# Kernel tuning notes

Measured on AMD Instinct MI355X. Metric: run time of the kernel, lower is better.

Reference implementation:

```python
import jax, jax.numpy as jnp
import numpy as np

N_NODES = 50000
N_EDGES = 300000
IN_FEATS = 128
N_HIDDEN = 64
N_HEADS = 4
N_CLASSES = 47
NEG_SLOPE = 0.2


def setup_inputs() -> dict:
    key = jax.random.key(0)
    ks = jax.random.split(key, 16)
    s = 0.1
    inp = {
        "x": jax.random.normal(ks[0], (N_NODES, IN_FEATS), jnp.float32),
        "src": jax.random.randint(ks[1], (N_EDGES,), 0, N_NODES, jnp.int64 if jax.config.jax_enable_x64 else jnp.int32),
        "dst": jax.random.randint(ks[2], (N_EDGES,), 0, N_NODES, jnp.int64 if jax.config.jax_enable_x64 else jnp.int32),
        # layer 1: in_feats -> (heads, hidden)
        "W1": jax.random.normal(ks[3], (IN_FEATS, N_HEADS * N_HIDDEN), jnp.float32) * s,
        "al1": jax.random.normal(ks[4], (N_HEADS, N_HIDDEN), jnp.float32) * s,
        "ar1": jax.random.normal(ks[5], (N_HEADS, N_HIDDEN), jnp.float32) * s,
        "b1": jnp.zeros((N_HEADS * N_HIDDEN,), jnp.float32),
        # layer 2: heads*hidden -> (heads, hidden)
        "W2": jax.random.normal(ks[6], (N_HEADS * N_HIDDEN, N_HEADS * N_HIDDEN), jnp.float32) * s,
        "al2": jax.random.normal(ks[7], (N_HEADS, N_HIDDEN), jnp.float32) * s,
        "ar2": jax.random.normal(ks[8], (N_HEADS, N_HIDDEN), jnp.float32) * s,
        "b2": jnp.zeros((N_HEADS * N_HIDDEN,), jnp.float32),
        # layer 3: heads*hidden -> (1, n_classes)
        "W3": jax.random.normal(ks[9], (N_HEADS * N_HIDDEN, N_CLASSES), jnp.float32) * s,
        "al3": jax.random.normal(ks[10], (1, N_CLASSES), jnp.float32) * s,
        "ar3": jax.random.normal(ks[11], (1, N_CLASSES), jnp.float32) * s,
        "b3": jnp.zeros((N_CLASSES,), jnp.float32),
    }
    return inp


def gat_conv(h, src, dst, W, al, ar, b, n_nodes):
    """DGL GATConv (shared src/dst projection, edge-softmax over dst)."""
    H, D = al.shape
    feat = (h @ W).reshape(n_nodes, H, D)              # [N,H,D]
    el = jnp.sum(feat * al[None], axis=-1)             # [N,H]
    er = jnp.sum(feat * ar[None], axis=-1)             # [N,H]
    e = jax.nn.leaky_relu(el[src] + er[dst], NEG_SLOPE)  # [E,H]
    emax = jax.ops.segment_max(e, dst, num_segments=n_nodes)  # [N,H]
    emax = jnp.where(jnp.isfinite(emax), emax, 0.0)    # empty segments
    ee = jnp.exp(e - emax[dst])                        # [E,H]
    denom = jax.ops.segment_sum(ee, dst, num_segments=n_nodes)  # [N,H]
    alpha = ee / jnp.maximum(denom[dst], 1e-9)         # [E,H]
    msg = feat[src] * alpha[..., None]                 # [E,H,D]
    out = jax.ops.segment_sum(msg, dst, num_segments=n_nodes)   # [N,H,D]
    return out + b.reshape(1, H, D)


def reference(x, src, dst, W1, al1, ar1, b1, W2, al2, ar2, b2, W3, al3, ar3, b3):
    n = x.shape[0]
    h = gat_conv(x, src, dst, W1, al1, ar1, b1, n).reshape(n, -1)  # flatten heads
    h = gat_conv(h, src, dst, W2, al2, ar2, b2, n).reshape(n, -1)
    h = gat_conv(h, src, dst, W3, al3, ar3, b3, n)                 # [N,1,C]
    return h.mean(axis=1)                                          # [N,C]
```

## Files before the change

### kernel.cpp

```cpp
#include <hip/hip_runtime.h>
#include <cstddef>

#define GAT_N 50000
#define GAT_E 300000
#define SCAN_B 256

typedef short bf16x8 __attribute__((ext_vector_type(8)));
typedef float f32x4  __attribute__((ext_vector_type(4)));
typedef unsigned int u32;

__device__ __forceinline__ ushort f2bf(float f) {
    unsigned u = __float_as_uint(f);
    return (ushort)((u + 0x7fffu + ((u >> 16) & 1u)) >> 16);
}
__device__ __forceinline__ float bf2f(ushort h) {
    return __uint_as_float((unsigned)h << 16);
}

__device__ __forceinline__ void gload16(const ushort* g, ushort* l) {
    __builtin_amdgcn_global_load_lds(
        (const __attribute__((address_space(1))) u32*)g,
        (__attribute__((address_space(3))) u32*)l, 16, 0, 0);
}


__global__ __launch_bounds__(256) void zero_ints(int* __restrict__ a, int n) {
    int i = blockIdx.x * blockDim.x + threadIdx.x;
    int stride = gridDim.x * blockDim.x;
    for (; i < n; i += stride) a[i] = 0;
}

__global__ __launch_bounds__(256) void count_k(
    const int* __restrict__ dst, int* __restrict__ cnt, int E)
{
    int e = blockIdx.x * blockDim.x + threadIdx.x;
    if (e < E) atomicAdd(&cnt[dst[e]], 1);
}

__global__ __launch_bounds__(256) void csr_partial(
    const int* __restrict__ cnt, int* __restrict__ partials, int N, int chunk)
{
    __shared__ int red[256];
    int b = blockIdx.x, t = threadIdx.x;
    int s = 0;
    for (int i = t; i < chunk; i += 256) {
        int idx = b * chunk + i;
        if (idx < N) s += cnt[idx];
    }
    red[t] = s;
    __syncthreads();
    for (int off = 128; off > 0; off >>= 1) {
        if (t < off) red[t] += red[t + off];
        __syncthreads();
    }
    if (t == 0) partials[b] = red[0];
}

__global__ __launch_bounds__(SCAN_B) void csr_scanp(
    int* __restrict__ partials, int* __restrict__ rowptr, int N)
{
    __shared__ int sc[SCAN_B];
    int t = threadIdx.x;
    int v = partials[t];
    sc[t] = v;
    __syncthreads();
    for (int off = 1; off < SCAN_B; off <<= 1) {
        int u = (t >= off) ? sc[t - off] : 0;
        __syncthreads();
        sc[t] += u;
        __syncthreads();
    }
    partials[t] = sc[t] - v;
    if (t == SCAN_B - 1) rowptr[N] = sc[t];
}

__global__ __launch_bounds__(256) void csr_write(
    const int* __restrict__ cnt, const int* __restrict__ partials,
    int* __restrict__ rowptr, int N, int chunk)
{
    __shared__ int sc[256];
    int b = blockIdx.x, t = threadIdx.x;
    int idx = b * chunk + t;
    int v = (t < chunk && idx < N) ? cnt[idx] : 0;
    sc[t] = v;
    __syncthreads();
    for (int off = 1; off < 256; off <<= 1) {
        int u = (t >= off) ? sc[t - off] : 0;
        __syncthreads();
        sc[t] += u;
        __syncthreads();
    }
    if (t < chunk && idx < N) rowptr[idx] = partials[b] + sc[t] - v;
}

__global__ __launch_bounds__(256) void scatter_k(
    const int* __restrict__ src, const int* __restrict__ dst,
    const int* __restrict__ rowptr, int* __restrict__ cursor,
    int* __restrict__ ssrc, int* __restrict__ sdst, int E)
{
    int e = blockIdx.x * blockDim.x + threadIdx.x;
    if (e >= E) return;
    int d = dst[e];
    int p = rowptr[d] + atomicAdd(&cursor[d], 1);
    ssrc[p] = src[e];
    sdst[p] = d;
}


__global__ __launch_bounds__(256) void convert_x(
    const float* __restrict__ x, ushort* __restrict__ Xh, ushort* __restrict__ Xl,
    long total4)
{
    long i = (long)blockIdx.x * blockDim.x + threadIdx.x;
    long stride = (long)gridDim.x * blockDim.x;
    for (; i < total4; i += stride) {
        float4 v = *(const float4*)(x + i * 4);
        ushort4 h, lo;
        h.x = f2bf(v.x); lo.x = f2bf(v.x - bf2f(h.x));
        h.y = f2bf(v.y); lo.y = f2bf(v.y - bf2f(h.y));
        h.z = f2bf(v.z); lo.z = f2bf(v.z - bf2f(h.z));
        h.w = f2bf(v.w); lo.w = f2bf(v.w - bf2f(h.w));
        *(ushort4*)(Xh + i * 4) = h;
        *(ushort4*)(Xl + i * 4) = lo;
    }
}

__global__ __launch_bounds__(256) void convert_w(
    const float* __restrict__ W, ushort* __restrict__ Wth, ushort* __restrict__ Wtl,
    int K, int M, int Mp)
{
    int idx = blockIdx.x * blockDim.x + threadIdx.x;
    if (idx >= Mp * K) return;
    int c = idx / K, k = idx - c * K;
    float v = (c < M) ? W[(size_t)k * M + c] : 0.f;
    ushort h = f2bf(v);
    Wth[idx] = h;
    Wtl[idx] = f2bf(v - bf2f(h));
}


__global__ __launch_bounds__(256) void gemm_feat(
    const ushort* __restrict__ Ah, const ushort* __restrict__ Al,
    const ushort* __restrict__ Wh, const ushort* __restrict__ Wl,
    const float* __restrict__ alw, const float* __restrict__ arw,
    float* __restrict__ feat, float* __restrict__ el, float* __restrict__ er,
    int N, int K, int M, int H, int D, int ldF)
{
    __shared__ ushort lds[2 * 16384];

    const int m0 = blockIdx.x * 128;
    const int n0 = blockIdx.y * 128;
    const int t = threadIdx.x;
    const int w = t >> 6, lane = t & 63;
    const int lr = lane & 15, lg = lane >> 4;
    const int wrb = (w >> 1) * 4;
    const int wcb = (w & 1) * 4;
    const int NK = K >> 5;

    const ushort* srcp[8];
    u32 lbase[8];
    #pragma unroll
    for (int l = 0; l < 8; ++l) {
        int ub = l * 256 + w * 64;
        int u = ub + lane;
        int region = u >> 9;
        int v = u & 511;
        int rowblk = v >> 6, kc = (v >> 4) & 3, rc = v & 15;
        const ushort* s;
        if (region < 2) {
            int grow = m0 + rowblk * 16 + rc;
            grow = grow < N ? grow : N - 1;
            s = (region ? Al : Ah) + (size_t)grow * K + kc * 8;
        } else {
            int gcol = n0 + rowblk * 16 + rc;
            s = ((region & 1) ? Wl : Wh) + (size_t)gcol * K + kc * 8;
        }
        srcp[l] = s;
        lbase[l] = (u32)(ub * 8);
    }

    f32x4 acc[4][4] = {};

    #pragma unroll
    for (int l = 0; l < 8; ++l) {
        gload16(srcp[l], &lds[lbase[l]]);
        srcp[l] += 32;
    }
    __syncthreads();

    int cur = 0;
    for (int kt = 0; kt < NK; ++kt) {
        if (kt + 1 < NK) {
            int nb = (cur ^ 1) * 16384;
            #pragma unroll
            for (int l = 0; l < 8; ++l) {
                gload16(srcp[l], &lds[nb + lbase[l]]);
                srcp[l] += 32;
            }
        }
        const ushort* buf = lds + cur * 16384;
        bf16x8 a_h[4], a_l[4];
        #pragma unroll
        for (int fi = 0; fi < 4; ++fi) {
            int aidx = ((wrb + fi) * 4 + lg) * 128 + lr * 8;
            a_h[fi] = *(const bf16x8*)&buf[aidx];
            a_l[fi] = *(const bf16x8*)&buf[4096 + aidx];
        }
        #pragma unroll
        for (int fj = 0; fj < 4; ++fj) {
            int bidx = ((wcb + fj) * 4 + lg) * 128 + lr * 8;
            bf16x8 b_h = *(const bf16x8*)&buf[8192 + bidx];
            bf16x8 b_l = *(const bf16x8*)&buf[12288 + bidx];
            #pragma unroll
            for (int fi = 0; fi < 4; ++fi) {
                acc[fi][fj] = __builtin_amdgcn_mfma_f32_16x16x32_bf16(a_h[fi], b_h, acc[fi][fj], 0, 0, 0);
                acc[fi][fj] = __builtin_amdgcn_mfma_f32_16x16x32_bf16(a_l[fi], b_h, acc[fi][fj], 0, 0, 0);
                acc[fi][fj] = __builtin_amdgcn_mfma_f32_16x16x32_bf16(a_h[fi], b_l, acc[fi][fj], 0, 0, 0);
            }
        }
        __syncthreads();
        cur ^= 1;
    }

    #pragma unroll
    for (int fi = 0; fi < 4; ++fi) {
        #pragma unroll
        for (int q = 0; q < 4; ++q) {
            int row = m0 + (w >> 1) * 64 + fi * 16 + 4 * lg + q;
            if (row < N) {
                #pragma unroll
                for (int fj = 0; fj < 4; ++fj) {
                    int col = n0 + (w & 1) * 64 + fj * 16 + lr;
                    if (col < M) feat[(size_t)row * ldF + col] = acc[fi][fj][q];
                }
            }
        }
    }

    const int head = (n0 + (w & 1) * 64) / D;
    if (head < H) {
        float alv[4], arv[4];
        #pragma unroll
        for (int fj = 0; fj < 4; ++fj) {
            int col = n0 + (w & 1) * 64 + fj * 16 + lr;
            alv[fj] = (col < M) ? alw[col] : 0.f;
            arv[fj] = (col < M) ? arw[col] : 0.f;
        }
        #pragma unroll
        for (int fi = 0; fi < 4; ++fi) {
            #pragma unroll
            for (int q = 0; q < 4; ++q) {
                float s1 = 0.f, s2 = 0.f;
                #pragma unroll
                for (int fj = 0; fj < 4; ++fj) {
                    s1 = fmaf(acc[fi][fj][q], alv[fj], s1);
                    s2 = fmaf(acc[fi][fj][q], arv[fj], s2);
                }
                #pragma unroll
                for (int mask = 1; mask <= 8; mask <<= 1) {
                    s1 += __shfl_xor(s1, mask);
                    s2 += __shfl_xor(s2, mask);
                }
                int row = m0 + (w >> 1) * 64 + fi * 16 + 4 * lg + q;
                if (lr == 0 && row < N) {
                    el[(size_t)row * H + head] = s1;
                    er[(size_t)row * H + head] = s2;
                }
            }
        }
    }
}


__global__ __launch_bounds__(256) void edge_score4(
    const int* __restrict__ ssrc, const int* __restrict__ sdst,
    const float* __restrict__ el, const float* __restrict__ er,
    float* __restrict__ sc, int E)
{
    int p = blockIdx.x * blockDim.x + threadIdx.x;
    if (p >= E) return;
    int s = ssrc[p], d = sdst[p];
    float4 a = *(const float4*)(el + (size_t)s * 4);
    float4 b = *(const float4*)(er + (size_t)d * 4);
    float4 v;
    v.x = a.x + b.x; v.x = v.x > 0.f ? v.x : 0.2f * v.x;
    v.y = a.y + b.y; v.y = v.y > 0.f ? v.y : 0.2f * v.y;
    v.z = a.z + b.z; v.z = v.z > 0.f ? v.z : 0.2f * v.z;
    v.w = a.w + b.w; v.w = v.w > 0.f ? v.w : 0.2f * v.w;
    *(float4*)(sc + (size_t)p * 4) = v;
}

__global__ __launch_bounds__(256) void edge_score1(
    const int* __restrict__ ssrc, const int* __restrict__ sdst,
    const float* __restrict__ el, const float* __restrict__ er,
    float* __restrict__ sc, int E)
{
    int p = blockIdx.x * blockDim.x + threadIdx.x;
    if (p >= E) return;
    float v = el[ssrc[p]] + er[sdst[p]];
    sc[p] = v > 0.f ? v : 0.2f * v;
}


__global__ __launch_bounds__(256) void node_aggr256(
    const int* __restrict__ rowptr, const int* __restrict__ ssrc,
    const float* __restrict__ sc, const float* __restrict__ feat,
    const float* __restrict__ bias,
    ushort* __restrict__ Ah_out, ushort* __restrict__ Al_out, int N)
{
    int wid = blockIdx.x * 4 + (threadIdx.x >> 6);
    int na = wid * 2;
    if (na >= N) return;
    int nb = na + 1;
    bool hb = nb < N;
    int lane = threadIdx.x & 63;
    int h = lane >> 4, sub = lane & 15;
    int begA = rowptr[na], endA = rowptr[na + 1];
    int begB = 0, endB = 0;
    if (hb) { begB = rowptr[nb]; endB = rowptr[nb + 1]; }

    float ma = -__builtin_inff(), mb = -__builtin_inff();
    for (int j = begA + sub; j < endA; j += 16) ma = fmaxf(ma, sc[(size_t)j * 4 + h]);
    for (int j = begB + sub; j < endB; j += 16) mb = fmaxf(mb, sc[(size_t)j * 4 + h]);
    #pragma unroll
    for (int mask = 1; mask <= 8; mask <<= 1) {
        ma = fmaxf(ma, __shfl_xor(ma, mask));
        mb = fmaxf(mb, __shfl_xor(mb, mask));
    }

    float dena = 0.f, denb = 0.f;
    for (int j = begA + sub; j < endA; j += 16) dena += __expf(sc[(size_t)j * 4 + h] - ma);
    for (int j = begB + sub; j < endB; j += 16) denb += __expf(sc[(size_t)j * 4 + h] - mb);
    #pragma unroll
    for (int mask = 1; mask <= 8; mask <<= 1) {
        dena += __shfl_xor(dena, mask);
        denb += __shfl_xor(denb, mask);
    }
    float invA = 1.f / fmaxf(dena, 1e-9f);
    float invB = 1.f / fmaxf(denb, 1e-9f);

    int degA = endA - begA, degB = endB - begB;
    int dmax = degA > degB ? degA : degB;

    float a0 = 0.f, a1 = 0.f, a2 = 0.f, a3 = 0.f;
    float b0 = 0.f, b1 = 0.f, b2 = 0.f, b3 = 0.f;
    for (int k = 0; k < dmax; k += 2) {
        bool v0 = k < degA,     v1 = k + 1 < degA;
        bool v2 = k < degB,     v3 = k + 1 < degB;
        int i0 = v0 ? begA + k     : 0;
        int i1 = v1 ? begA + k + 1 : 0;
        int i2 = v2 ? begB + k     : 0;
        int i3 = v3 ? begB + k + 1 : 0;
        int s0 = ssrc[i0], s1 = ssrc[i1], s2 = ssrc[i2], s3 = ssrc[i3];
        float w0 = v0 ? __expf(sc[(size_t)i0 * 4 + h] - ma) : 0.f;
        float w1 = v1 ? __expf(sc[(size_t)i1 * 4 + h] - ma) : 0.f;
        float w2 = v2 ? __expf(sc[(size_t)i2 * 4 + h] - mb) : 0.f;
        float w3 = v3 ? __expf(sc[(size_t)i3 * 4 + h] - mb) : 0.f;
        float4 f0 = *(const float4*)(feat + (size_t)s0 * 256 + lane * 4);
        float4 f1 = *(const float4*)(feat + (size_t)s1 * 256 + lane * 4);
        float4 f2 = *(const float4*)(feat + (size_t)s2 * 256 + lane * 4);
        float4 f3 = *(const float4*)(feat + (size_t)s3 * 256 + lane * 4);
        a0 = fmaf(w0, f0.x, fmaf(w1, f1.x, a0));
        a1 = fmaf(w0, f0.y, fmaf(w1, f1.y, a1));
        a2 = fmaf(w0, f0.z, fmaf(w1, f1.z, a2));
        a3 = fmaf(w0, f0.w, fmaf(w1, f1.w, a3));
        b0 = fmaf(w2, f2.x, fmaf(w3, f3.x, b0));
        b1 = fmaf(w2, f2.y, fmaf(w3, f3.y, b1));
        b2 = fmaf(w2, f2.z, fmaf(w3, f3.z, b2));
        b3 = fmaf(w2, f2.w, fmaf(w3, f3.w, b3));
    }

    float bs0 = bias[lane * 4 + 0], bs1 = bias[lane * 4 + 1];
    float bs2 = bias[lane * 4 + 2], bs3 = bias[lane * 4 + 3];
    {
        float v0 = fmaf(a0, invA, bs0), v1 = fmaf(a1, invA, bs1);
        float v2 = fmaf(a2, invA, bs2), v3 = fmaf(a3, invA, bs3);
        ushort4 hh, lo;
        hh.x = f2bf(v0); lo.x = f2bf(v0 - bf2f(hh.x));
        hh.y = f2bf(v1); lo.y = f2bf(v1 - bf2f(hh.y));
        hh.z = f2bf(v2); lo.z = f2bf(v2 - bf2f(hh.z));
        hh.w = f2bf(v3); lo.w = f2bf(v3 - bf2f(hh.w));
        *(ushort4*)(Ah_out + (size_t)na * 256 + lane * 4) = hh;
        *(ushort4*)(Al_out + (size_t)na * 256 + lane * 4) = lo;
    }
    if (hb) {
        float v0 = fmaf(b0, invB, bs0), v1 = fmaf(b1, invB, bs1);
        float v2 = fmaf(b2, invB, bs2), v3 = fmaf(b3, invB, bs3);
        ushort4 hh, lo;
        hh.x = f2bf(v0); lo.x = f2bf(v0 - bf2f(hh.x));
        hh.y = f2bf(v1); lo.y = f2bf(v1 - bf2f(hh.y));
        hh.z = f2bf(v2); lo.z = f2bf(v2 - bf2f(hh.z));
        hh.w = f2bf(v3); lo.w = f2bf(v3 - bf2f(hh.w));
        *(ushort4*)(Ah_out + (size_t)nb * 256 + lane * 4) = hh;
        *(ushort4*)(Al_out + (size_t)nb * 256 + lane * 4) = lo;
    }
}

__global__ __launch_bounds__(256) void node_aggr47(
    const int* __restrict__ rowptr, const int* __restrict__ ssrc,
    const float* __restrict__ sc, const float* __restrict__ feat,
    const float* __restrict__ bias, float* __restrict__ out, int N)
{
    int n = blockIdx.x * 4 + (threadIdx.x >> 6);
    if (n >= N) return;
    int lane = threadIdx.x & 63;
    int beg = rowptr[n], end = rowptr[n + 1];

    float m = -__builtin_inff();
    for (int j = beg + lane; j < end; j += 64)
        m = fmaxf(m, sc[j]);
    #pragma unroll
    for (int mask = 1; mask <= 32; mask <<= 1)
        m = fmaxf(m, __shfl_xor(m, mask));

    float denom = 0.f;
    for (int j = beg + lane; j < end; j += 64)
        denom += __expf(sc[j] - m);
    #pragma unroll
    for (int mask = 1; mask <= 32; mask <<= 1)
        denom += __shfl_xor(denom, mask);

    float inv = 1.f / fmaxf(denom, 1e-9f);
    float acc = 0.f;
    int j = beg;
    for (; j + 4 <= end; j += 4) {
        int s0 = ssrc[j + 0], s1 = ssrc[j + 1], s2 = ssrc[j + 2], s3 = ssrc[j + 3];
        float w0 = __expf(sc[j + 0] - m);
        float w1 = __expf(sc[j + 1] - m);
        float w2 = __expf(sc[j + 2] - m);
        float w3 = __expf(sc[j + 3] - m);
        float f0 = (lane < 47) ? feat[(size_t)s0 * 48 + lane] : 0.f;
        float f1 = (lane < 47) ? feat[(size_t)s1 * 48 + lane] : 0.f;
        float f2 = (lane < 47) ? feat[(size_t)s2 * 48 + lane] : 0.f;
        float f3 = (lane < 47) ? feat[(size_t)s3 * 48 + lane] : 0.f;
        acc = fmaf(w0, f0, fmaf(w1, f1, fmaf(w2, f2, fmaf(w3, f3, acc))));
    }
    for (; j < end; ++j) {
        float wgt = __expf(sc[j] - m);
        int s = ssrc[j];
        float f = (lane < 47) ? feat[(size_t)s * 48 + lane] : 0.f;
        acc = fmaf(wgt, f, acc);
    }
    if (lane < 47)
        out[(size_t)n * 47 + lane] = fmaf(acc, inv, bias[lane]);
}


extern "C" void kernel_launch(void* const* d_in, const int* in_sizes, int n_in,
                              void* d_out, int out_size, void* d_ws, size_t ws_size,
                              hipStream_t stream) {
    const float* x   = (const float*)d_in[0];
    const int*   src = (const int*)d_in[1];
    const int*   dst = (const int*)d_in[2];
    const float* W1  = (const float*)d_in[3];
    const float* al1 = (const float*)d_in[4];
    const float* ar1 = (const float*)d_in[5];
    const float* b1  = (const float*)d_in[6];
    const float* W2  = (const float*)d_in[7];
    const float* al2 = (const float*)d_in[8];
    const float* ar2 = (const float*)d_in[9];
    const float* b2  = (const float*)d_in[10];
    const float* W3  = (const float*)d_in[11];
    const float* al3 = (const float*)d_in[12];
    const float* ar3 = (const float*)d_in[13];
    const float* b3  = (const float*)d_in[14];
    float* out = (float*)d_out;

    const int N = GAT_N, E = GAT_E;
    const int chunk = (N + SCAN_B - 1) / SCAN_B;

    char* wsb = (char*)d_ws;
    size_t o = 0;
    float*  feat  = (float*)(wsb + o);  o += (size_t)N * 256 * 4;
    ushort* Ah    = (ushort*)(wsb + o); o += (size_t)N * 256 * 2;
    ushort* Al    = (ushort*)(wsb + o); o += (size_t)N * 256 * 2;
    float*  el    = (float*)(wsb + o);  o += (size_t)N * 4 * 4;
    float*  er    = (float*)(wsb + o);  o += (size_t)N * 4 * 4;
    int* rowptr   = (int*)(wsb + o);    o += (size_t)(N + 1) * 4;
    int* cnt      = (int*)(wsb + o);    o += (size_t)N * 4;
    int* cursor   = (int*)(wsb + o);    o += (size_t)N * 4;
    int* ssrc     = (int*)(wsb + o);    o += (size_t)E * 4;
    int* sdst     = (int*)(wsb + o);    o += (size_t)E * 4;
    float* scbuf  = (float*)(wsb + o);  o += (size_t)E * 4 * 4;
    int* partials = (int*)(wsb + o);    o += (size_t)SCAN_B * 4;
    ushort* Wt1h  = (ushort*)(wsb + o); o += (size_t)256 * 128 * 2;
    ushort* Wt1l  = (ushort*)(wsb + o); o += (size_t)256 * 128 * 2;
    ushort* Wt2h  = (ushort*)(wsb + o); o += (size_t)256 * 256 * 2;
    ushort* Wt2l  = (ushort*)(wsb + o); o += (size_t)256 * 256 * 2;
    ushort* Wt3h  = (ushort*)(wsb + o); o += (size_t)128 * 256 * 2;
    ushort* Wt3l  = (ushort*)(wsb + o); o += (size_t)128 * 256 * 2;
    ushort* Xh = Ah;
    ushort* Xl = Al;

    dim3 blk(256);
    int gE = (E + 255) / 256;
    int gN = (N + 3) / 4;
    int gN2 = ((N + 1) / 2 + 3) / 4;
    dim3 gemmG((N + 127) / 128, 2);
    dim3 gemmG3((N + 127) / 128, 1);

    zero_ints<<<64, blk, 0, stream>>>(cnt, 2 * N);
    count_k<<<gE, blk, 0, stream>>>(dst, cnt, E);
    csr_partial<<<SCAN_B, blk, 0, stream>>>(cnt, partials, N, chunk);
    csr_scanp<<<1, SCAN_B, 0, stream>>>(partials, rowptr, N);
    csr_write<<<SCAN_B, blk, 0, stream>>>(cnt, partials, rowptr, N, chunk);
    scatter_k<<<gE, blk, 0, stream>>>(src, dst, rowptr, cursor, ssrc, sdst, E);

    convert_x<<<2048, blk, 0, stream>>>(x, Xh, Xl, (long)N * 128 / 4);
    convert_w<<<(256 * 128 + 255) / 256, blk, 0, stream>>>(W1, Wt1h, Wt1l, 128, 256, 256);
    convert_w<<<(256 * 256 + 255) / 256, blk, 0, stream>>>(W2, Wt2h, Wt2l, 256, 256, 256);
    convert_w<<<(128 * 256 + 255) / 256, blk, 0, stream>>>(W3, Wt3h, Wt3l, 256, 47, 128);

    gemm_feat<<<gemmG, blk, 0, stream>>>(Xh, Xl, Wt1h, Wt1l, al1, ar1,
                                         feat, el, er, N, 128, 256, 4, 64, 256);
    edge_score4<<<gE, blk, 0, stream>>>(ssrc, sdst, el, er, scbuf, E);
    node_aggr256<<<gN2, blk, 0, stream>>>(rowptr, ssrc, scbuf, feat, b1, Ah, Al, N);

    gemm_feat<<<gemmG, blk, 0, stream>>>(Ah, Al, Wt2h, Wt2l, al2, ar2,
                                         feat, el, er, N, 256, 256, 4, 64, 256);
    edge_score4<<<gE, blk, 0, stream>>>(ssrc, sdst, el, er, scbuf, E);
    node_aggr256<<<gN2, blk, 0, stream>>>(rowptr, ssrc, scbuf, feat, b2, Ah, Al, N);

    gemm_feat<<<gemmG3, blk, 0, stream>>>(Ah, Al, Wt3h, Wt3l, al3, ar3,
                                          feat, el, er, N, 256, 47, 1, 47, 48);
    edge_score1<<<gE, blk, 0, stream>>>(ssrc, sdst, el, er, scbuf, E);
    node_aggr47<<<gN, blk, 0, stream>>>(rowptr, ssrc, scbuf, feat, b3, out, N);
}
```

Before: 326.5 us.

## Restructure GAT GEMM: A rows in registers, full-width W tiles in LDS

The feature GEMM is rewritten as a templated kernel. Each block handles 64 rows and all output columns: each wave keeps its 16 A rows for the whole K dimension in registers, and W k-slices are streamed through single-buffered LDS. Layer 3 now computes only 48 padded columns instead of 128, and the el/er reductions over all heads happen in one pass. This removes the column-split grid, which re-read A for each column block, and drops wasted MFMA work on padding. In exchange it needs more registers and loses double buffering, adding two barriers per k-step.

```diff
diff --git a/kernel.cpp b/kernel.cpp
--- a/kernel.cpp
+++ b/kernel.cpp
@@ -139,133 +139,105 @@
 }
 
 
+template<int NK, int NC, int HH>
 __global__ __launch_bounds__(256) void gemm_feat(
     const ushort* __restrict__ Ah, const ushort* __restrict__ Al,
     const ushort* __restrict__ Wh, const ushort* __restrict__ Wl,
     const float* __restrict__ alw, const float* __restrict__ arw,
     float* __restrict__ feat, float* __restrict__ el, float* __restrict__ er,
-    int N, int K, int M, int H, int D, int ldF)
-{
-    __shared__ ushort lds[2 * 16384];
-
-    const int m0 = blockIdx.x * 128;
-    const int n0 = blockIdx.y * 128;
-    const int t = threadIdx.x;
-    const int w = t >> 6, lane = t & 63;
+    int N, int M, int ldF)
+{
+    constexpr int K = NK * 32;
+    constexpr int CH = NC * 64;
+    constexpr int TOT = CH * 2;
+    constexpr int LPT = (TOT + 255) / 256;
+    constexpr int CBH = NC / HH;
+    __shared__ ushort lds[NC * 1024];
+
+    const int m0 = blockIdx.x * 64;
+    const int t = threadIdx.x, w = t >> 6, lane = t & 63;
     const int lr = lane & 15, lg = lane >> 4;
-    const int wrb = (w >> 1) * 4;
-    const int wcb = (w & 1) * 4;
-    const int NK = K >> 5;
-
-    const ushort* srcp[8];
-    u32 lbase[8];
-    #pragma unroll
-    for (int l = 0; l < 8; ++l) {
+
+    int arow = m0 + w * 16 + lr;
+    if (arow > N - 1) arow = N - 1;
+    bf16x8 areg_h[NK], areg_l[NK];
+    #pragma unroll
+    for (int kc = 0; kc < NK; ++kc) {
+        areg_h[kc] = *(const bf16x8*)(Ah + (size_t)arow * K + kc * 32 + lg * 8);
+        areg_l[kc] = *(const bf16x8*)(Al + (size_t)arow * K + kc * 32 + lg * 8);
+    }
+
+    const ushort* srcp[LPT];
+    int ubs[LPT];
+    #pragma unroll
+    for (int l = 0; l < LPT; ++l) {
         int ub = l * 256 + w * 64;
+        ubs[l] = ub;
         int u = ub + lane;
-        int region = u >> 9;
-        int v = u & 511;
-        int rowblk = v >> 6, kc = (v >> 4) & 3, rc = v & 15;
-        const ushort* s;
-        if (region < 2) {
-            int grow = m0 + rowblk * 16 + rc;
-            grow = grow < N ? grow : N - 1;
-            s = (region ? Al : Ah) + (size_t)grow * K + kc * 8;
-        } else {
-            int gcol = n0 + rowblk * 16 + rc;
-            s = ((region & 1) ? Wl : Wh) + (size_t)gcol * K + kc * 8;
+        int uu = (u < TOT) ? u : 0;
+        int reg = (uu >= CH) ? 1 : 0;
+        int v = uu - reg * CH;
+        int cb = v >> 6, kc2 = (v >> 4) & 3, c = v & 15;
+        srcp[l] = (reg ? Wl : Wh) + (size_t)(cb * 16 + c) * K + kc2 * 8;
+    }
+
+    f32x4 acc[NC] = {};
+
+    #pragma unroll
+    for (int l = 0; l < LPT; ++l)
+        if (ubs[l] < TOT) { gload16(srcp[l], &lds[ubs[l] * 8]); srcp[l] += 32; }
+    __syncthreads();
+
+    #pragma unroll
+    for (int s = 0; s < NK; ++s) {
+        #pragma unroll
+        for (int cb = 0; cb < NC; ++cb) {
+            bf16x8 b_h = *(const bf16x8*)&lds[(cb * 4 + lg) * 128 + lr * 8];
+            bf16x8 b_l = *(const bf16x8*)&lds[NC * 512 + (cb * 4 + lg) * 128 + lr * 8];
+            acc[cb] = __builtin_amdgcn_mfma_f32_16x16x32_bf16(areg_h[s], b_h, acc[cb], 0, 0, 0);
+            acc[cb] = __builtin_amdgcn_mfma_f32_16x16x32_bf16(areg_l[s], b_h, acc[cb], 0, 0, 0);
+            acc[cb] = __builtin_amdgcn_mfma_f32_16x16x32_bf16(areg_h[s], b_l, acc[cb], 0, 0, 0);
         }
-        srcp[l] = s;
-        lbase[l] = (u32)(ub * 8);
-    }
-
-    f32x4 acc[4][4] = {};
-
-    #pragma unroll
-    for (int l = 0; l < 8; ++l) {
-        gload16(srcp[l], &lds[lbase[l]]);
-        srcp[l] += 32;
-    }
-    __syncthreads();
-
-    int cur = 0;
-    for (int kt = 0; kt < NK; ++kt) {
-        if (kt + 1 < NK) {
-            int nb = (cur ^ 1) * 16384;
+        if (s + 1 < NK) {
+            __syncthreads();
             #pragma unroll
-            for (int l = 0; l < 8; ++l) {
-                gload16(srcp[l], &lds[nb + lbase[l]]);
-                srcp[l] += 32;
-            }
+            for (int l = 0; l < LPT; ++l)
+                if (ubs[l] < TOT) { gload16(srcp[l], &lds[ubs[l] * 8]); srcp[l] += 32; }
+            __syncthreads();
         }
-        const ushort* buf = lds + cur * 16384;
-        bf16x8 a_h[4], a_l[4];
+    }
+
+    float alv[NC], arv[NC];
+    #pragma unroll
+    for (int cb = 0; cb < NC; ++cb) {
+        int col = cb * 16 + lr;
+        alv[cb] = (col < M) ? alw[col] : 0.f;
+        arv[cb] = (col < M) ? arw[col] : 0.f;
+    }
+    #pragma unroll
+    for (int q = 0; q < 4; ++q) {
+        int row = m0 + w * 16 + 4 * lg + q;
+        bool rok = row < N;
+        float s1[HH], s2[HH];
         #pragma unroll
-        for (int fi = 0; fi < 4; ++fi) {
-            int aidx = ((wrb + fi) * 4 + lg) * 128 + lr * 8;
-            a_h[fi] = *(const bf16x8*)&buf[aidx];
-            a_l[fi] = *(const bf16x8*)&buf[4096 + aidx];
+        for (int hh = 0; hh < HH; ++hh) { s1[hh] = 0.f; s2[hh] = 0.f; }
+        #pragma unroll
+        for (int cb = 0; cb < NC; ++cb) {
+            int col = cb * 16 + lr;
+            if (rok && col < M) feat[(size_t)row * ldF + col] = acc[cb][q];
+            s1[cb / CBH] = fmaf(acc[cb][q], alv[cb], s1[cb / CBH]);
+            s2[cb / CBH] = fmaf(acc[cb][q], arv[cb], s2[cb / CBH]);
         }
         #pragma unroll
-        for (int fj = 0; fj < 4; ++fj) {
-            int bidx = ((wcb + fj) * 4 + lg) * 128 + lr * 8;
-            bf16x8 b_h = *(const bf16x8*)&buf[8192 + bidx];
-            bf16x8 b_l = *(const bf16x8*)&buf[12288 + bidx];
+        for (int hh = 0; hh < HH; ++hh) {
             #pragma unroll
-            for (int fi = 0; fi < 4; ++fi) {
-                acc[fi][fj] = __builtin_amdgcn_mfma_f32_16x16x32_bf16(a_h[fi], b_h, acc[fi][fj], 0, 0, 0);
-                acc[fi][fj] = __builtin_amdgcn_mfma_f32_16x16x32_bf16(a_l[fi], b_h, acc[fi][fj], 0, 0, 0);
-                acc[fi][fj] = __builtin_amdgcn_mfma_f32_16x16x32_bf16(a_h[fi], b_l, acc[fi][fj], 0, 0, 0);
+            for (int mask = 1; mask <= 8; mask <<= 1) {
+                s1[hh] += __shfl_xor(s1[hh], mask);
+                s2[hh] += __shfl_xor(s2[hh], mask);
             }
-        }
-        __syncthreads();
-        cur ^= 1;
-    }
-
-    #pragma unroll
-    for (int fi = 0; fi < 4; ++fi) {
-        #pragma unroll
-        for (int q = 0; q < 4; ++q) {
-            int row = m0 + (w >> 1) * 64 + fi * 16 + 4 * lg + q;
-            if (row < N) {
-                #pragma unroll
-                for (int fj = 0; fj < 4; ++fj) {
-                    int col = n0 + (w & 1) * 64 + fj * 16 + lr;
-                    if (col < M) feat[(size_t)row * ldF + col] = acc[fi][fj][q];
-                }
-            }
-        }
-    }
-
-    const int head = (n0 + (w & 1) * 64) / D;
-    if (head < H) {
-        float alv[4], arv[4];
-        #pragma unroll
-        for (int fj = 0; fj < 4; ++fj) {
-            int col = n0 + (w & 1) * 64 + fj * 16 + lr;
-            alv[fj] = (col < M) ? alw[col] : 0.f;
-            arv[fj] = (col < M) ? arw[col] : 0.f;
-        }
-        #pragma unroll
-        for (int fi = 0; fi < 4; ++fi) {
-            #pragma unroll
-            for (int q = 0; q < 4; ++q) {
-                float s1 = 0.f, s2 = 0.f;
-                #pragma unroll
-                for (int fj = 0; fj < 4; ++fj) {
-                    s1 = fmaf(acc[fi][fj][q], alv[fj], s1);
-                    s2 = fmaf(acc[fi][fj][q], arv[fj], s2);
-                }
-                #pragma unroll
-                for (int mask = 1; mask <= 8; mask <<= 1) {
-                    s1 += __shfl_xor(s1, mask);
-                    s2 += __shfl_xor(s2, mask);
-                }
-                int row = m0 + (w >> 1) * 64 + fi * 16 + 4 * lg + q;
-                if (lr == 0 && row < N) {
-                    el[(size_t)row * H + head] = s1;
-                    er[(size_t)row * H + head] = s2;
-                }
+            if (lr == 0 && rok) {
+                el[(size_t)row * HH + hh] = s1[hh];
+                er[(size_t)row * HH + hh] = s2[hh];
             }
         }
     }
@@ -487,8 +459,8 @@
     ushort* Wt1l  = (ushort*)(wsb + o); o += (size_t)256 * 128 * 2;
     ushort* Wt2h  = (ushort*)(wsb + o); o += (size_t)256 * 256 * 2;
     ushort* Wt2l  = (ushort*)(wsb + o); o += (size_t)256 * 256 * 2;
-    ushort* Wt3h  = (ushort*)(wsb + o); o += (size_t)128 * 256 * 2;
-    ushort* Wt3l  = (ushort*)(wsb + o); o += (size_t)128 * 256 * 2;
+    ushort* Wt3h  = (ushort*)(wsb + o); o += (size_t)48 * 256 * 2;
+    ushort* Wt3l  = (ushort*)(wsb + o); o += (size_t)48 * 256 * 2;
     ushort* Xh = Ah;
     ushort* Xl = Al;
 
@@ -496,8 +468,7 @@
     int gE = (E + 255) / 256;
     int gN = (N + 3) / 4;
     int gN2 = ((N + 1) / 2 + 3) / 4;
-    dim3 gemmG((N + 127) / 128, 2);
-    dim3 gemmG3((N + 127) / 128, 1);
+    int gG = (N + 63) / 64;
 
     zero_ints<<<64, blk, 0, stream>>>(cnt, 2 * N);
     count_k<<<gE, blk, 0, stream>>>(dst, cnt, E);
@@ -509,20 +480,20 @@
     convert_x<<<2048, blk, 0, stream>>>(x, Xh, Xl, (long)N * 128 / 4);
     convert_w<<<(256 * 128 + 255) / 256, blk, 0, stream>>>(W1, Wt1h, Wt1l, 128, 256, 256);
     convert_w<<<(256 * 256 + 255) / 256, blk, 0, stream>>>(W2, Wt2h, Wt2l, 256, 256, 256);
-    convert_w<<<(128 * 256 + 255) / 256, blk, 0, stream>>>(W3, Wt3h, Wt3l, 256, 47, 128);
-
-    gemm_feat<<<gemmG, blk, 0, stream>>>(Xh, Xl, Wt1h, Wt1l, al1, ar1,
-                                         feat, el, er, N, 128, 256, 4, 64, 256);
+    convert_w<<<(48 * 256 + 255) / 256, blk, 0, stream>>>(W3, Wt3h, Wt3l, 256, 47, 48);
+
+    gemm_feat<4, 16, 4><<<gG, blk, 0, stream>>>(Xh, Xl, Wt1h, Wt1l, al1, ar1,
+                                                feat, el, er, N, 256, 256);
     edge_score4<<<gE, blk, 0, stream>>>(ssrc, sdst, el, er, scbuf, E);
     node_aggr256<<<gN2, blk, 0, stream>>>(rowptr, ssrc, scbuf, feat, b1, Ah, Al, N);
 
-    gemm_feat<<<gemmG, blk, 0, stream>>>(Ah, Al, Wt2h, Wt2l, al2, ar2,
-                                         feat, el, er, N, 256, 256, 4, 64, 256);
+    gemm_feat<8, 16, 4><<<gG, blk, 0, stream>>>(Ah, Al, Wt2h, Wt2l, al2, ar2,
+                                                feat, el, er, N, 256, 256);
     edge_score4<<<gE, blk, 0, stream>>>(ssrc, sdst, el, er, scbuf, E);
     node_aggr256<<<gN2, blk, 0, stream>>>(rowptr, ssrc, scbuf, feat, b2, Ah, Al, N);
 
-    gemm_feat<<<gemmG3, blk, 0, stream>>>(Ah, Al, Wt3h, Wt3l, al3, ar3,
-                                          feat, el, er, N, 256, 47, 1, 47, 48);
+    gemm_feat<8, 3, 1><<<gG, blk, 0, stream>>>(Ah, Al, Wt3h, Wt3l, al3, ar3,
+                                               feat, el, er, N, 47, 48);
     edge_score1<<<gE, blk, 0, stream>>>(ssrc, sdst, el, er, scbuf, E);
     node_aggr47<<<gN, blk, 0, stream>>>(rowptr, ssrc, scbuf, feat, b3, out, N);
 }
```

After: 328.8 us. About the same (+0.7%).

## Shrink GEMM row tile to 64 and use explicit vmcnt waits with raw barriers

Applied to the files above, without the earlier changes.

The feature-projection GEMM now uses 64-row tiles instead of 128, which halves the per-wave accumulator set and LDS footprint and doubles the grid size for better occupancy and load balance. The single __syncthreads per K-step is replaced by explicit s_waitcnt vmcnt plus s_barrier with sched_barriers, so the prefetch of the next tile can stay in flight while the current one is consumed. The cost is less B-tile reuse per block, so weight traffic per output row goes up.

```diff
diff --git a/kernel.cpp b/kernel.cpp
--- a/kernel.cpp
+++ b/kernel.cpp
@@ -146,108 +146,114 @@
     float* __restrict__ feat, float* __restrict__ el, float* __restrict__ er,
     int N, int K, int M, int H, int D, int ldF)
 {
-    __shared__ ushort lds[2 * 16384];
-
-    const int m0 = blockIdx.x * 128;
+    __shared__ ushort lds[2 * 12288];
+
+    const int m0 = blockIdx.x * 64;
     const int n0 = blockIdx.y * 128;
     const int t = threadIdx.x;
     const int w = t >> 6, lane = t & 63;
     const int lr = lane & 15, lg = lane >> 4;
-    const int wrb = (w >> 1) * 4;
-    const int wcb = (w & 1) * 4;
+    const int wr = (w >> 1) * 32, wc = (w & 1) * 64;
     const int NK = K >> 5;
 
-    const ushort* srcp[8];
-    u32 lbase[8];
-    #pragma unroll
-    for (int l = 0; l < 8; ++l) {
+    const ushort* srcp[6];
+    u32 lbase[6];
+    #pragma unroll
+    for (int l = 0; l < 6; ++l) {
         int ub = l * 256 + w * 64;
         int u = ub + lane;
-        int region = u >> 9;
-        int v = u & 511;
-        int rowblk = v >> 6, kc = (v >> 4) & 3, rc = v & 15;
         const ushort* s;
-        if (region < 2) {
-            int grow = m0 + rowblk * 16 + rc;
+        if (u < 512) {
+            int half = u >> 8;
+            int v = u & 255;
+            int rowblk = v >> 6, kc = (v >> 4) & 3, r = v & 15;
+            int grow = m0 + rowblk * 16 + r;
             grow = grow < N ? grow : N - 1;
-            s = (region ? Al : Ah) + (size_t)grow * K + kc * 8;
+            s = (half ? Al : Ah) + (size_t)grow * K + kc * 8;
         } else {
-            int gcol = n0 + rowblk * 16 + rc;
-            s = ((region & 1) ? Wl : Wh) + (size_t)gcol * K + kc * 8;
+            int v = u - 512;
+            int half = v >> 9;
+            int b = v & 511;
+            int cb = b >> 6, kc = (b >> 4) & 3, c = b & 15;
+            int gcol = n0 + cb * 16 + c;
+            s = (half ? Wl : Wh) + (size_t)gcol * K + kc * 8;
         }
         srcp[l] = s;
         lbase[l] = (u32)(ub * 8);
     }
 
-    f32x4 acc[4][4] = {};
-
-    #pragma unroll
-    for (int l = 0; l < 8; ++l) {
-        gload16(srcp[l], &lds[lbase[l]]);
-        srcp[l] += 32;
-    }
-    __syncthreads();
+    f32x4 acc[2][4] = {};
+
+    #pragma unroll
+    for (int l = 0; l < 6; ++l) { gload16(srcp[l], &lds[lbase[l]]); srcp[l] += 32; }
 
     int cur = 0;
     for (int kt = 0; kt < NK; ++kt) {
         if (kt + 1 < NK) {
-            int nb = (cur ^ 1) * 16384;
+            int nb = (cur ^ 1) * 12288;
             #pragma unroll
-            for (int l = 0; l < 8; ++l) {
-                gload16(srcp[l], &lds[nb + lbase[l]]);
-                srcp[l] += 32;
-            }
-        }
-        const ushort* buf = lds + cur * 16384;
-        bf16x8 a_h[4], a_l[4];
+            for (int l = 0; l < 6; ++l) { gload16(srcp[l], &lds[nb + lbase[l]]); srcp[l] += 32; }
+            asm volatile("s_waitcnt vmcnt(6)" ::: "memory");
+        } else {
+            asm volatile("s_waitcnt vmcnt(0)" ::: "memory");
+        }
+        __builtin_amdgcn_sched_barrier(0);
+        __builtin_amdgcn_s_barrier();
+        __builtin_amdgcn_sched_barrier(0);
+
+        const ushort* buf = lds + cur * 12288;
+        const int rb = (w >> 1) * 2;
+        const int cbb = (w & 1) * 4;
+        bf16x8 a_h[2], a_l[2];
         #pragma unroll
-        for (int fi = 0; fi < 4; ++fi) {
-            int aidx = ((wrb + fi) * 4 + lg) * 128 + lr * 8;
-            a_h[fi] = *(const bf16x8*)&buf[aidx];
-            a_l[fi] = *(const bf16x8*)&buf[4096 + aidx];
+        for (int fi = 0; fi < 2; ++fi) {
+            int idx = ((rb + fi) * 4 + lg) * 128 + lr * 8;
+            a_h[fi] = *(const bf16x8*)&buf[idx];
+            a_l[fi] = *(const bf16x8*)&buf[2048 + idx];
         }
         #pragma unroll
         for (int fj = 0; fj < 4; ++fj) {
-            int bidx = ((wcb + fj) * 4 + lg) * 128 + lr * 8;
-            bf16x8 b_h = *(const bf16x8*)&buf[8192 + bidx];
-            bf16x8 b_l = *(const bf16x8*)&buf[12288 + bidx];
+            int idx = ((cbb + fj) * 4 + lg) * 128 + lr * 8;
+            bf16x8 b_h = *(const bf16x8*)&buf[4096 + idx];
+            bf16x8 b_l = *(const bf16x8*)&buf[8192 + idx];
             #pragma unroll
-            for (int fi = 0; fi < 4; ++fi) {
+            for (int fi = 0; fi < 2; ++fi) {
                 acc[fi][fj] = __builtin_amdgcn_mfma_f32_16x16x32_bf16(a_h[fi], b_h, acc[fi][fj], 0, 0, 0);
                 acc[fi][fj] = __builtin_amdgcn_mfma_f32_16x16x32_bf16(a_l[fi], b_h, acc[fi][fj], 0, 0, 0);
                 acc[fi][fj] = __builtin_amdgcn_mfma_f32_16x16x32_bf16(a_h[fi], b_l, acc[fi][fj], 0, 0, 0);
             }
         }
-        __syncthreads();
+        __builtin_amdgcn_sched_barrier(0);
+        __builtin_amdgcn_s_barrier();
         cur ^= 1;
     }
 
     #pragma unroll
-    for (int fi = 0; fi < 4; ++fi) {
+    for (int fi = 0; fi < 2; ++fi) {
         #pragma unroll
         for (int q = 0; q < 4; ++q) {
-            int row = m0 + (w >> 1) * 64 + fi * 16 + 4 * lg + q;
+            int row = m0 + wr + fi * 16 + 4 * lg + q;
             if (row < N) {
                 #pragma unroll
                 for (int fj = 0; fj < 4; ++fj) {
-                    int col = n0 + (w & 1) * 64 + fj * 16 + lr;
+                    int col = n0 + wc + fj * 16 + lr;
                     if (col < M) feat[(size_t)row * ldF + col] = acc[fi][fj][q];
                 }
             }
         }
     }
 
-    const int head = (n0 + (w & 1) * 64) / D;
+    const int head = (n0 + wc) / D;
     if (head < H) {
         float alv[4], arv[4];
         #pragma unroll
         for (int fj = 0; fj < 4; ++fj) {
-            int col = n0 + (w & 1) * 64 + fj * 16 + lr;
+            int col = n0 + wc + fj * 16 + lr;
             alv[fj] = (col < M) ? alw[col] : 0.f;
             arv[fj] = (col < M) ? arw[col] : 0.f;
         }
         #pragma unroll
-        for (int fi = 0; fi < 4; ++fi) {
+        for (int fi = 0; fi < 2; ++fi) {
             #pragma unroll
             for (int q = 0; q < 4; ++q) {
                 float s1 = 0.f, s2 = 0.f;
@@ -261,7 +267,7 @@
                     s1 += __shfl_xor(s1, mask);
                     s2 += __shfl_xor(s2, mask);
                 }
-                int row = m0 + (w >> 1) * 64 + fi * 16 + 4 * lg + q;
+                int row = m0 + wr + fi * 16 + 4 * lg + q;
                 if (lr == 0 && row < N) {
                     el[(size_t)row * H + head] = s1;
                     er[(size_t)row * H + head] = s2;
@@ -496,8 +502,8 @@
     int gE = (E + 255) / 256;
     int gN = (N + 3) / 4;
     int gN2 = ((N + 1) / 2 + 3) / 4;
-    dim3 gemmG((N + 127) / 128, 2);
-    dim3 gemmG3((N + 127) / 128, 1);
+    dim3 gemmG((N + 63) / 64, 2);
+    dim3 gemmG3((N + 63) / 64, 1);
 
     zero_ints<<<64, blk, 0, stream>>>(cnt, 2 * N);
     count_k<<<gE, blk, 0, stream>>>(dst, cnt, E);
```

New measurement: 326.9 us. No clear change (+0.1%).
